# Kernel optimization log

Measured on AMD Instinct MI355X. Metric: run time of the kernel, lower is better.

## Reference

```python
import jax, jax.numpy as jnp
import numpy as np

EMBED = 1024
HEADS = 16
HDIM = EMBED // HEADS
B, S = 4, 2048
NEG = -1e20


def setup_inputs() -> dict:
    key = jax.random.key(0)
    ks = jax.random.split(key, 9)
    query = jax.random.normal(ks[0], (B, S, EMBED), dtype=jnp.float32)
    key_t = jax.random.normal(ks[1], (B, S, EMBED), dtype=jnp.float32)
    value = jax.random.normal(ks[2], (B, S, EMBED), dtype=jnp.float32)
    mask = jax.random.randint(ks[3], (1, 1, S, S), 0, 2, dtype=jnp.int32)
    padding = jax.random.randint(ks[4], (B, 1, 1, S), 0, 2, dtype=jnp.int32)
    sc = 1.0 / np.sqrt(EMBED)
    Wq = jax.random.normal(ks[5], (EMBED, EMBED), dtype=jnp.float32) * sc
    Wk = jax.random.normal(ks[6], (EMBED, EMBED), dtype=jnp.float32) * sc
    Wv = jax.random.normal(ks[7], (EMBED, EMBED), dtype=jnp.float32) * sc
    Wo = jax.random.normal(ks[8], (EMBED, EMBED), dtype=jnp.float32) * sc
    return {"query": query, "key": key_t, "value": value, "mask": mask,
            "padding": padding, "Wq": Wq, "Wk": Wk, "Wv": Wv, "Wo": Wo}


def reference(query, key, value, mask, padding, Wq, Wk, Wv, Wo):
    b, q_len, _ = query.shape
    k_len = key.shape[1]
    # projections (nn.Linear: x @ W^T), split into heads
    qs = (query @ Wq.T).reshape(b, q_len, HEADS, HDIM)
    ks = (key @ Wk.T).reshape(b, k_len, HEADS, HDIM)
    vs = (value @ Wv.T).reshape(b, k_len, HEADS, HDIM)
    scale = EMBED ** 0.25
    qs = qs / scale
    ks = ks / scale
    # [b, h, q, k] scores
    dot = jnp.einsum('bkhd,bqhd->bhqk', ks, qs)
    dot = jnp.where(mask == 0, NEG, dot)
    dot = jnp.where(padding == 0, NEG, dot)
    attn = jax.nn.softmax(dot, axis=-1)
    alpha = jnp.einsum('bhqk,bkhd->bqhd', attn, vs)
    out = alpha.reshape(b, q_len, EMBED) @ Wo.T
    return out
```

## Files before the change

### kernel.cpp

```cpp
#include <hip/hip_runtime.h>
#include <stdint.h>

#define B_  4
#define S_  2048
#define E_  1024
#define H_  16
#define D_  64

typedef __bf16 bf16;
typedef __bf16 bf16x4 __attribute__((ext_vector_type(4)));
typedef __bf16 bf16x8 __attribute__((ext_vector_type(8)));
typedef float  f32x4 __attribute__((ext_vector_type(4)));
typedef float  f32x16 __attribute__((ext_vector_type(16)));
typedef uint32_t u32x4 __attribute__((ext_vector_type(4)));

__device__ __forceinline__ f32x4 mfma16(bf16x8 a, bf16x8 b, f32x4 c) {
  return __builtin_amdgcn_mfma_f32_16x16x32_bf16(a, b, c, 0, 0, 0);
}
__device__ __forceinline__ f32x16 mfma32(bf16x8 a, bf16x8 b, f32x16 c) {
  return __builtin_amdgcn_mfma_f32_32x32x16_bf16(a, b, c, 0, 0, 0);
}

__device__ __forceinline__ int sw(int row, int idx) { return idx ^ ((row & 7) << 3); }

__device__ __forceinline__ void gl_lds16(const void* g, void* l) {
  __builtin_amdgcn_global_load_lds(
      (const __attribute__((address_space(1))) void*)g,
      (__attribute__((address_space(3))) void*)l, 16, 0, 0);
}

__device__ __forceinline__ uint32_t cvtpk(float lo, float hi) {
  uint32_t r;
  asm("v_cvt_pk_bf16_f32 %0, %1, %2" : "=v"(r) : "v"(lo), "v"(hi));
  return r;
}
__device__ __forceinline__ void plswap(uint32_t& a, uint32_t& b) {
  asm("v_permlane32_swap_b32 %0, %1" : "+v"(a), "+v"(b));
}

__global__ void pack_mask_kernel(const int* __restrict__ mask, uint32_t* __restrict__ mbits) {
  int idx = blockIdx.x * 256 + threadIdx.x;
  int q = idx >> 6, w = idx & 63;
  const int* p = mask + q * S_ + w * 32;
  uint32_t bits = 0;
#pragma unroll
  for (int j = 0; j < 32; j += 4) {
    int4 v = *(const int4*)(p + j);
    bits |= (v.x != 0 ? 1u : 0u) << (j + 0);
    bits |= (v.y != 0 ? 1u : 0u) << (j + 1);
    bits |= (v.z != 0 ? 1u : 0u) << (j + 2);
    bits |= (v.w != 0 ? 1u : 0u) << (j + 3);
  }
  mbits[idx] = bits;
}

__global__ void pack_pad_kernel(const int* __restrict__ pad, uint32_t* __restrict__ pbits) {
  int idx = threadIdx.x;
  int b = idx >> 6, w = idx & 63;
  const int* p = pad + b * S_ + w * 32;
  uint32_t bits = 0;
#pragma unroll
  for (int j = 0; j < 32; j += 4) {
    int4 v = *(const int4*)(p + j);
    bits |= (v.x != 0 ? 1u : 0u) << (j + 0);
    bits |= (v.y != 0 ? 1u : 0u) << (j + 1);
    bits |= (v.z != 0 ? 1u : 0u) << (j + 2);
    bits |= (v.w != 0 ? 1u : 0u) << (j + 3);
  }
  pbits[idx] = bits;
}

__global__ __launch_bounds__(256)
void expand_mask(const uint32_t* __restrict__ mbits, const uint32_t* __restrict__ pbits,
                 uint2* __restrict__ mbt) {
  int idx = blockIdx.x * 256 + threadIdx.x;
  int q = idx & 2047;
  int kt = (idx >> 11) & 31;
  int b = idx >> 16;
  uint2 r;
  r.x = mbits[q * 64 + kt * 2 + 0] & pbits[b * 64 + kt * 2 + 0];
  r.y = mbits[q * 64 + kt * 2 + 1] & pbits[b * 64 + kt * 2 + 1];
  mbt[idx] = r;
}

__global__ __launch_bounds__(256)
void cvt_act(const float* __restrict__ q, const float* __restrict__ k,
             const float* __restrict__ v, bf16* __restrict__ out) {
  const float* src = blockIdx.z == 0 ? q : (blockIdx.z == 1 ? k : v);
  size_t i = ((size_t)blockIdx.x * 256 + threadIdx.x) * 8;
  float4 a = *(const float4*)(src + i);
  float4 b = *(const float4*)(src + i + 4);
  bf16x8 o;
  o[0] = (bf16)a.x; o[1] = (bf16)a.y; o[2] = (bf16)a.z; o[3] = (bf16)a.w;
  o[4] = (bf16)b.x; o[5] = (bf16)b.y; o[6] = (bf16)b.z; o[7] = (bf16)b.w;
  *(bf16x8*)(out + (size_t)blockIdx.z * (8192ull * 1024ull) + i) = o;
}

__global__ __launch_bounds__(256)
void cvt_w(const float* __restrict__ w0, const float* __restrict__ w1,
           const float* __restrict__ w2, const float* __restrict__ w3,
           bf16* __restrict__ out, float sq, float sk) {
  int z = blockIdx.z;
  const float* src = z == 0 ? w0 : (z == 1 ? w1 : (z == 2 ? w2 : w3));
  float s = (z == 0) ? sq : ((z == 1) ? sk : 1.0f);
  size_t i = ((size_t)blockIdx.x * 256 + threadIdx.x) * 8;
  float4 a = *(const float4*)(src + i);
  float4 b = *(const float4*)(src + i + 4);
  bf16x8 o;
  o[0] = (bf16)(a.x * s); o[1] = (bf16)(a.y * s); o[2] = (bf16)(a.z * s); o[3] = (bf16)(a.w * s);
  o[4] = (bf16)(b.x * s); o[5] = (bf16)(b.y * s); o[6] = (bf16)(b.z * s); o[7] = (bf16)(b.w * s);
  *(bf16x8*)(out + (size_t)z * (1024ull * 1024ull) + i) = o;
}

struct GA { const bf16* A; const bf16* W; void* O; };

template<bool OUT_F32>
__global__ __launch_bounds__(256, 4)
void gemm_bf(GA g0, GA g1, GA g2) {
  GA g = (blockIdx.z == 0) ? g0 : ((blockIdx.z == 1) ? g1 : g2);
  const int id = blockIdx.x;
  const int brow = ((id & 7) * 8 + (id >> 6)) * 128;
  const int bcol = ((id >> 3) & 7) * 128;
  const int tid = threadIdx.x;
  const int l = tid & 63, wv = tid >> 6;
  const int lg = l >> 4, lr = l & 15;
  const int wr = wv >> 1, wc = wv & 1;
  const int sr = l >> 3, sc8 = l & 7;

  __shared__ bf16 Ls[2][128 * 64];
  bf16* As = Ls[0];
  bf16* Bs = Ls[1];

  f32x4 acc[4][4] = {};

  const bf16* Ab = g.A + (size_t)(brow + wv * 32 + sr) * E_ + (size_t)(sc8 ^ sr) * 8;
  const bf16* Bb = g.W + (size_t)(bcol + wv * 32 + sr) * E_ + (size_t)(sc8 ^ sr) * 8;
  bf16* la = As + (wv * 32) * 64;
  bf16* lb = Bs + (wv * 32) * 64;

  for (int kt = 0; kt < E_ / 64; ++kt) {
    __syncthreads();
    const bf16* a = Ab + kt * 64;
    const bf16* b = Bb + kt * 64;
#pragma unroll
    for (int i = 0; i < 4; ++i) {
      gl_lds16(a + (size_t)i * 8 * E_, la + i * 8 * 64);
      gl_lds16(b + (size_t)i * 8 * E_, lb + i * 8 * 64);
    }
    __syncthreads();
#pragma unroll
    for (int kk = 0; kk < 2; ++kk) {
      bf16x8 af[4], bfr[4];
#pragma unroll
      for (int ms = 0; ms < 4; ++ms) {
        int row = wr * 64 + ms * 16 + lr;
        af[ms] = *(const bf16x8*)&As[sw(row, row * 64 + kk * 32 + lg * 8)];
      }
#pragma unroll
      for (int ns = 0; ns < 4; ++ns) {
        int row = wc * 64 + ns * 16 + lr;
        bfr[ns] = *(const bf16x8*)&Bs[sw(row, row * 64 + kk * 32 + lg * 8)];
      }
#pragma unroll
      for (int ms = 0; ms < 4; ++ms)
#pragma unroll
        for (int ns = 0; ns < 4; ++ns)
          acc[ms][ns] = mfma16(af[ms], bfr[ns], acc[ms][ns]);
    }
  }

  if (!OUT_F32 && blockIdx.z == 2) {
    bf16* T = &Ls[0][0];
    __syncthreads();
#pragma unroll
    for (int ms = 0; ms < 4; ++ms) {
#pragma unroll
      for (int ns = 0; ns < 4; ++ns) {
        int col = wc * 64 + ns * 16 + lr;
        int rowb = wr * 64 + ms * 16 + lg * 4;
        bf16x4 hv;
#pragma unroll
        for (int r = 0; r < 4; ++r) hv[r] = (bf16)acc[ms][ns][r];
        *(bf16x4*)&T[col * 128 + (rowb ^ ((col & 7) << 3))] = hv;
      }
    }
    __syncthreads();
    int chunk = tid & 15, dl0 = tid >> 4;
#pragma unroll
    for (int pass = 0; pass < 8; ++pass) {
      int dl = pass * 16 + dl0;
      bf16x8 v = *(const bf16x8*)&T[dl * 128 + ((chunk * 8) ^ ((dl & 7) << 3))];
      int colg = bcol + dl;
      int bh2 = (brow >> 11) * 16 + (colg >> 6);
      int d = colg & 63;
      int s0 = (brow & 2047) + chunk * 8;
      *(bf16x8*)((bf16*)g.O + ((size_t)bh2 * 64 + d) * (size_t)S_ + s0) = v;
    }
    return;
  }

#pragma unroll
  for (int ms = 0; ms < 4; ++ms) {
#pragma unroll
    for (int ns = 0; ns < 4; ++ns) {
#pragma unroll
      for (int r = 0; r < 4; ++r) {
        int row = brow + wr * 64 + ms * 16 + lg * 4 + r;
        int col = bcol + wc * 64 + ns * 16 + lr;
        if constexpr (OUT_F32) ((float*)g.O)[(size_t)row * E_ + col] = acc[ms][ns][r];
        else                   ((bf16*)g.O)[(size_t)row * E_ + col] = (bf16)acc[ms][ns][r];
      }
    }
  }
}

__global__ __launch_bounds__(256, 4)
void attn_kernel(const bf16* __restrict__ Q, const bf16* __restrict__ K,
                 const bf16* __restrict__ Vt, const uint2* __restrict__ mbt,
                 bf16* __restrict__ alpha) {
  const int raw = blockIdx.x;
  const int xcd = raw & 7, slot = raw >> 3;
  const int bh = xcd * 8 + (slot >> 4), qblk = slot & 15;
  const int b = bh >> 4, h = bh & 15;
  const int tid = threadIdx.x, wv = tid >> 6, l = tid & 63;
  const int ln = l & 31, hi = l >> 5;
  const int qw = qblk * 128 + wv * 32;
  const int sr = l >> 3, sc8 = l & 7;
  const int g = (ln & 7) ^ (ln >> 3);

  __shared__ bf16 Ks[2][64 * 64];
  __shared__ bf16 Vs[2][64 * 64];

  bf16x8 qreg[4];
#pragma unroll
  for (int dc = 0; dc < 4; ++dc)
    qreg[dc] = *(const bf16x8*)(Q + (size_t)(b * S_ + qw + ln) * E_ + h * 64 + dc * 16 + hi * 8);

  bf16x8 ones;
#pragma unroll
  for (int j = 0; j < 8; ++j) ones[j] = (bf16)1.0f;

  f32x16 o[2] = {};
  f32x16 lacc = {};

  const bf16* Kb = K + (size_t)b * S_ * E_ + (size_t)h * 64;
  const bf16* Vb = Vt + (size_t)bh * 64 * S_;
  const uint2* mrow = mbt + ((size_t)b << 16) + qw + ln;

  auto stage = [&](int buf, int kt) {
#pragma unroll
    for (int op = 0; op < 2; ++op) {
      int rb = wv * 16 + op * 8;
      int cK = (sc8 ^ sr ^ ((rb >> 3) & 7)) * 8;
      gl_lds16(Kb + (size_t)(kt * 64 + rb + sr) * E_ + cK, Ks[buf] + rb * 64);
      gl_lds16(Vb + (size_t)(rb + sr) * S_ + kt * 64 + cK, Vs[buf] + rb * 64);
    }
  };

  stage(0, 0);
  __syncthreads();

  for (int kt = 0; kt < S_ / 64; ++kt) {
    const int cur = kt & 1;
    if (kt + 1 < S_ / 64) stage(cur ^ 1, kt + 1);

    f32x16 sc[2] = {};
    __builtin_amdgcn_s_setprio(1);
#pragma unroll
    for (int ct = 0; ct < 2; ++ct) {
#pragma unroll
      for (int dc = 0; dc < 4; ++dc) {
        int row = ct * 32 + ln;
        int c = (dc * 2 + hi) ^ g ^ (ct * 4);
        bf16x8 kf = *(const bf16x8*)&Ks[cur][row * 64 + c * 8];
        sc[ct] = mfma32(kf, qreg[dc], sc[ct]);
      }
    }
    __builtin_amdgcn_s_setprio(0);

    uint2 mv = mrow[kt << 11];
    uint32_t mq[2];
    mq[0] = mv.x >> (hi * 4);
    mq[1] = mv.y >> (hi * 4);

    uint32_t up[16];
#pragma unroll
    for (int ct = 0; ct < 2; ++ct) {
      float p[16];
#pragma unroll
      for (int r = 0; r < 16; ++r) {
        const int rel = (r & 3) + 8 * (r >> 2);
        float pe = __builtin_amdgcn_exp2f(sc[ct][r]);
        uint32_t keep = (uint32_t)__builtin_amdgcn_sbfe(mq[ct], rel, 1);
        p[r] = __builtin_bit_cast(float, __builtin_bit_cast(uint32_t, pe) & keep);
      }
#pragma unroll
      for (int j = 0; j < 8; ++j)
        up[ct * 8 + j] = cvtpk(p[2 * j], p[2 * j + 1]);
    }

#pragma unroll
    for (int kc = 0; kc < 4; ++kc) {
      const int ct = kc >> 1, base = ct * 8 + (kc & 1) * 4;
      plswap(up[base + 0], up[base + 2]);
      plswap(up[base + 1], up[base + 3]);
      u32x4 w = {up[base + 0], up[base + 1], up[base + 2], up[base + 3]};
      bf16x8 pf = __builtin_bit_cast(bf16x8, w);
      __builtin_amdgcn_s_setprio(1);
#pragma unroll
      for (int dt = 0; dt < 2; ++dt) {
        int row = dt * 32 + ln;
        int c = (kc * 2 + hi) ^ g ^ (dt * 4);
        bf16x8 vf = *(const bf16x8*)&Vs[cur][row * 64 + c * 8];
        o[dt] = mfma32(vf, pf, o[dt]);
      }
      lacc = mfma32(ones, pf, lacc);
      __builtin_amdgcn_s_setprio(0);
    }
    __syncthreads();
  }

  float inv = 1.0f / lacc[0];
  size_t qoff = (size_t)(b * S_ + qw + ln) * E_ + h * 64;
#pragma unroll
  for (int dt = 0; dt < 2; ++dt) {
#pragma unroll
    for (int rg = 0; rg < 4; ++rg) {
      bf16x4 ov;
#pragma unroll
      for (int j = 0; j < 4; ++j) ov[j] = (bf16)(o[dt][rg * 4 + j] * inv);
      *(bf16x4*)(alpha + qoff + dt * 32 + rg * 8 + hi * 4) = ov;
    }
  }
}

extern "C" void kernel_launch(void* const* d_in, const int* in_sizes, int n_in,
                              void* d_out, int out_size, void* d_ws, size_t ws_size,
                              hipStream_t stream) {
  const float* query = (const float*)d_in[0];
  const float* key_t = (const float*)d_in[1];
  const float* value = (const float*)d_in[2];
  const int*   mask  = (const int*)d_in[3];
  const int*   pad   = (const int*)d_in[4];
  const float* Wq    = (const float*)d_in[5];
  const float* Wk    = (const float*)d_in[6];
  const float* Wv    = (const float*)d_in[7];
  const float* Wo    = (const float*)d_in[8];

  char* ws = (char*)d_ws;
  bf16* Abuf  = (bf16*)ws;
  bf16* alpha = (bf16*)(ws + ((size_t)16 << 20));
  bf16* Wb    = (bf16*)(ws + ((size_t)48 << 20));
  bf16* QKV   = (bf16*)(ws + ((size_t)56 << 20));
  uint32_t* mbits = (uint32_t*)(ws + ((size_t)104 << 20));
  uint32_t* pbits = mbits + (size_t)S_ * 64;
  uint2*    mbt   = (uint2*)(ws + ((size_t)105 << 20));

  const size_t AM = 8192ull * 1024ull;
  const size_t WM = 1024ull * 1024ull;
  bf16* Vt = QKV + 2 * AM;

  pack_mask_kernel<<<512, 256, 0, stream>>>(mask, mbits);
  pack_pad_kernel<<<1, 256, 0, stream>>>(pad, pbits);
  expand_mask<<<1024, 256, 0, stream>>>(mbits, pbits, mbt);

  cvt_act<<<dim3(4096, 1, 3), 256, 0, stream>>>(query, key_t, value, Abuf);
  const float qscale = 0.17677669529663687f;
  const float log2e  = 1.4426950408889634f;
  cvt_w<<<dim3(512, 1, 4), 256, 0, stream>>>(Wq, Wk, Wv, Wo, Wb, qscale * log2e, qscale);

  GA gq{Abuf,          Wb,          QKV};
  GA gk{Abuf + AM,     Wb + WM,     QKV + AM};
  GA gv{Abuf + 2 * AM, Wb + 2 * WM, Vt};
  gemm_bf<false><<<dim3(512, 1, 3), 256, 0, stream>>>(gq, gk, gv);

  attn_kernel<<<1024, 256, 0, stream>>>(QKV, QKV + AM, Vt, mbt, alpha);

  GA go{alpha, Wb + 3 * WM, d_out};
  gemm_bf<true><<<dim3(512, 1, 1), 256, 0, stream>>>(go, go, go);
}
```

Measured before the change: 222.6 us.

## Fuse fp32-to-bf16 activation cast into QKV GEMM and split-K attention across two wave groups

Removes the separate cvt_act pass. The QKV GEMM now loads fp32 activations straight into LDS and packs them to bf16 in registers, which saves a full read and write of the bf16 copy. Attention blocks grow to 512 threads: two groups of 4 waves each handle half of the key range with 32-key tiles, and their partial outputs and row sums are combined through LDS at the end. The mask is repacked per 32-key word, and the ones-MFMA row sum is replaced by a scalar sum plus shuffle. The trade-offs are doubled LDS traffic for fp32 A tiles, lower GEMM occupancy (3 blocks), and an extra combine step.

```diff
diff --git a/kernel.cpp b/kernel.cpp
--- a/kernel.cpp
+++ b/kernel.cpp
@@ -72,28 +72,12 @@
 
 __global__ __launch_bounds__(256)
 void expand_mask(const uint32_t* __restrict__ mbits, const uint32_t* __restrict__ pbits,
-                 uint2* __restrict__ mbt) {
+                 uint32_t* __restrict__ mbt) {
   int idx = blockIdx.x * 256 + threadIdx.x;
   int q = idx & 2047;
-  int kt = (idx >> 11) & 31;
-  int b = idx >> 16;
-  uint2 r;
-  r.x = mbits[q * 64 + kt * 2 + 0] & pbits[b * 64 + kt * 2 + 0];
-  r.y = mbits[q * 64 + kt * 2 + 1] & pbits[b * 64 + kt * 2 + 1];
-  mbt[idx] = r;
-}
-
-__global__ __launch_bounds__(256)
-void cvt_act(const float* __restrict__ q, const float* __restrict__ k,
-             const float* __restrict__ v, bf16* __restrict__ out) {
-  const float* src = blockIdx.z == 0 ? q : (blockIdx.z == 1 ? k : v);
-  size_t i = ((size_t)blockIdx.x * 256 + threadIdx.x) * 8;
-  float4 a = *(const float4*)(src + i);
-  float4 b = *(const float4*)(src + i + 4);
-  bf16x8 o;
-  o[0] = (bf16)a.x; o[1] = (bf16)a.y; o[2] = (bf16)a.z; o[3] = (bf16)a.w;
-  o[4] = (bf16)b.x; o[5] = (bf16)b.y; o[6] = (bf16)b.z; o[7] = (bf16)b.w;
-  *(bf16x8*)(out + (size_t)blockIdx.z * (8192ull * 1024ull) + i) = o;
+  int ktw = (idx >> 11) & 63;
+  int b = idx >> 17;
+  mbt[idx] = mbits[q * 64 + ktw] & pbits[b * 64 + ktw];
 }
 
 __global__ __launch_bounds__(256)
@@ -112,10 +96,10 @@
   *(bf16x8*)(out + (size_t)z * (1024ull * 1024ull) + i) = o;
 }
 
-struct GA { const bf16* A; const bf16* W; void* O; };
-
-template<bool OUT_F32>
-__global__ __launch_bounds__(256, 4)
+struct GA { const void* A; const bf16* W; void* O; };
+
+template<bool A_F32, bool OUT_F32>
+__global__ __launch_bounds__(256, A_F32 ? 3 : 4)
 void gemm_bf(GA g0, GA g1, GA g2) {
   GA g = (blockIdx.z == 0) ? g0 : ((blockIdx.z == 1) ? g1 : g2);
   const int id = blockIdx.x;
@@ -125,27 +109,50 @@
   const int l = tid & 63, wv = tid >> 6;
   const int lg = l >> 4, lr = l & 15;
   const int wr = wv >> 1, wc = wv & 1;
+
+  __shared__ __align__(16) char smem[A_F32 ? 49152 : 32768];
+  bf16* Bs = (bf16*)(smem + (A_F32 ? 32768 : 16384));
+
+  f32x4 acc[4][4] = {};
+
   const int sr = l >> 3, sc8 = l & 7;
-
-  __shared__ bf16 Ls[2][128 * 64];
-  bf16* As = Ls[0];
-  bf16* Bs = Ls[1];
-
-  f32x4 acc[4][4] = {};
-
-  const bf16* Ab = g.A + (size_t)(brow + wv * 32 + sr) * E_ + (size_t)(sc8 ^ sr) * 8;
   const bf16* Bb = g.W + (size_t)(bcol + wv * 32 + sr) * E_ + (size_t)(sc8 ^ sr) * 8;
-  bf16* la = As + (wv * 32) * 64;
   bf16* lb = Bs + (wv * 32) * 64;
+
+  float* Asf = (float*)smem;
+  bf16*  Asb = (bf16*)smem;
+  const float* AbE = nullptr; const float* AbO = nullptr;
+  const bf16*  Abb = nullptr;
+  const int sr4 = l >> 4, sc16 = l & 15;
+  if constexpr (A_F32) {
+    const float* Af = (const float*)g.A;
+    AbE = Af + (size_t)(brow + wv * 32 + sr4) * E_ + (size_t)((sc16 ^ sr4) * 4);
+    AbO = Af + (size_t)(brow + wv * 32 + sr4) * E_ + (size_t)((sc16 ^ (4 + sr4)) * 4);
+  } else {
+    Abb = (const bf16*)g.A + (size_t)(brow + wv * 32 + sr) * E_ + (size_t)(sc8 ^ sr) * 8;
+  }
 
   for (int kt = 0; kt < E_ / 64; ++kt) {
     __syncthreads();
-    const bf16* a = Ab + kt * 64;
-    const bf16* b = Bb + kt * 64;
-#pragma unroll
-    for (int i = 0; i < 4; ++i) {
-      gl_lds16(a + (size_t)i * 8 * E_, la + i * 8 * 64);
-      gl_lds16(b + (size_t)i * 8 * E_, lb + i * 8 * 64);
+    if constexpr (A_F32) {
+      float* la = Asf + (wv * 32) * 64;
+#pragma unroll
+      for (int i = 0; i < 8; ++i) {
+        const float* src = ((i & 1) ? AbO : AbE) + (size_t)(i * 4) * E_ + kt * 64;
+        gl_lds16(src, la + (i * 4) * 64);
+      }
+    } else {
+      bf16* la = Asb + (wv * 32) * 64;
+      const bf16* a = Abb + kt * 64;
+#pragma unroll
+      for (int i = 0; i < 4; ++i)
+        gl_lds16(a + (size_t)i * 8 * E_, la + i * 8 * 64);
+    }
+    {
+      const bf16* b = Bb + kt * 64;
+#pragma unroll
+      for (int i = 0; i < 4; ++i)
+        gl_lds16(b + (size_t)i * 8 * E_, lb + i * 8 * 64);
     }
     __syncthreads();
 #pragma unroll
@@ -154,7 +161,16 @@
 #pragma unroll
       for (int ms = 0; ms < 4; ++ms) {
         int row = wr * 64 + ms * 16 + lr;
-        af[ms] = *(const bf16x8*)&As[sw(row, row * 64 + kk * 32 + lg * 8)];
+        if constexpr (A_F32) {
+          int g0c = 2 * (kk * 4 + lg);
+          f32x4 lo  = *(const f32x4*)&Asf[row * 64 + ((g0c ^ (row & 7)) * 4)];
+          f32x4 hi4 = *(const f32x4*)&Asf[row * 64 + (((g0c + 1) ^ (row & 7)) * 4)];
+          u32x4 pk = { cvtpk(lo[0], lo[1]), cvtpk(lo[2], lo[3]),
+                       cvtpk(hi4[0], hi4[1]), cvtpk(hi4[2], hi4[3]) };
+          af[ms] = __builtin_bit_cast(bf16x8, pk);
+        } else {
+          af[ms] = *(const bf16x8*)&Asb[sw(row, row * 64 + kk * 32 + lg * 8)];
+        }
       }
 #pragma unroll
       for (int ns = 0; ns < 4; ++ns) {
@@ -170,7 +186,7 @@
   }
 
   if (!OUT_F32 && blockIdx.z == 2) {
-    bf16* T = &Ls[0][0];
+    bf16* T = (bf16*)smem;
     __syncthreads();
 #pragma unroll
     for (int ms = 0; ms < 4; ++ms) {
@@ -214,9 +230,9 @@
   }
 }
 
-__global__ __launch_bounds__(256, 4)
+__global__ __launch_bounds__(512, 6)
 void attn_kernel(const bf16* __restrict__ Q, const bf16* __restrict__ K,
-                 const bf16* __restrict__ Vt, const uint2* __restrict__ mbt,
+                 const bf16* __restrict__ Vt, const uint32_t* __restrict__ mbt,
                  bf16* __restrict__ alpha) {
   const int raw = blockIdx.x;
   const int xcd = raw & 7, slot = raw >> 3;
@@ -224,84 +240,81 @@
   const int b = bh >> 4, h = bh & 15;
   const int tid = threadIdx.x, wv = tid >> 6, l = tid & 63;
   const int ln = l & 31, hi = l >> 5;
-  const int qw = qblk * 128 + wv * 32;
-  const int sr = l >> 3, sc8 = l & 7;
-  const int g = (ln & 7) ^ (ln >> 3);
-
-  __shared__ bf16 Ks[2][64 * 64];
-  __shared__ bf16 Vs[2][64 * 64];
+  const int grp = wv >> 2, wq = wv & 3;
+  const int qw = qblk * 128 + wq * 32;
+
+  __shared__ __align__(16) char smem[37888];
+  bf16* KsB = (bf16*)smem;
+  bf16* VsB = (bf16*)(smem + 16384);
+  float* comb = (float*)smem;
+  float* lsum = (float*)(smem + 36864);
 
   bf16x8 qreg[4];
 #pragma unroll
   for (int dc = 0; dc < 4; ++dc)
     qreg[dc] = *(const bf16x8*)(Q + (size_t)(b * S_ + qw + ln) * E_ + h * 64 + dc * 16 + hi * 8);
 
-  bf16x8 ones;
-#pragma unroll
-  for (int j = 0; j < 8; ++j) ones[j] = (bf16)1.0f;
-
   f32x16 o[2] = {};
-  f32x16 lacc = {};
+  float lrun = 0.f;
 
   const bf16* Kb = K + (size_t)b * S_ * E_ + (size_t)h * 64;
   const bf16* Vb = Vt + (size_t)bh * 64 * S_;
-  const uint2* mrow = mbt + ((size_t)b << 16) + qw + ln;
-
-  auto stage = [&](int buf, int kt) {
-#pragma unroll
-    for (int op = 0; op < 2; ++op) {
-      int rb = wv * 16 + op * 8;
-      int cK = (sc8 ^ sr ^ ((rb >> 3) & 7)) * 8;
-      gl_lds16(Kb + (size_t)(kt * 64 + rb + sr) * E_ + cK, Ks[buf] + rb * 64);
-      gl_lds16(Vb + (size_t)(rb + sr) * S_ + kt * 64 + cK, Vs[buf] + rb * 64);
-    }
+  const uint32_t* mrow = mbt + ((size_t)b << 17) + (qw + ln);
+
+  const int ksr = l >> 3, ksc = l & 7;
+  const int vsr = l >> 2, vsc = l & 3;
+  const int kr = wq * 8 + ksr;
+  const int dr = wq * 16 + vsr;
+
+  const bf16* Ksrc = Kb + (size_t)(grp * 1024 + kr) * E_ + (ksc ^ ksr) * 8;
+  const bf16* Vsrc = Vb + (size_t)dr * S_ + grp * 1024 + ((vsc ^ (vsr & 3)) * 8);
+
+  auto stage = [&](int buf, int t) {
+    gl_lds16(Ksrc + (size_t)(t * 32) * E_, KsB + (grp * 2 + buf) * 2048 + (wq * 8) * 64);
+    gl_lds16(Vsrc + t * 32,               VsB + (grp * 2 + buf) * 2048 + (wq * 16) * 32);
   };
 
   stage(0, 0);
   __syncthreads();
 
-  for (int kt = 0; kt < S_ / 64; ++kt) {
-    const int cur = kt & 1;
-    if (kt + 1 < S_ / 64) stage(cur ^ 1, kt + 1);
-
-    f32x16 sc[2] = {};
+  for (int t = 0; t < 32; ++t) {
+    const int cur = t & 1;
+    if (t + 1 < 32) stage(cur ^ 1, t + 1);
+    const bf16* ks = KsB + (grp * 2 + cur) * 2048;
+    const bf16* vs = VsB + (grp * 2 + cur) * 2048;
+
+    f32x16 sc = {};
     __builtin_amdgcn_s_setprio(1);
 #pragma unroll
-    for (int ct = 0; ct < 2; ++ct) {
-#pragma unroll
-      for (int dc = 0; dc < 4; ++dc) {
-        int row = ct * 32 + ln;
-        int c = (dc * 2 + hi) ^ g ^ (ct * 4);
-        bf16x8 kf = *(const bf16x8*)&Ks[cur][row * 64 + c * 8];
-        sc[ct] = mfma32(kf, qreg[dc], sc[ct]);
-      }
+    for (int dc = 0; dc < 4; ++dc) {
+      bf16x8 kf = *(const bf16x8*)&ks[ln * 64 + (((dc * 2 + hi) ^ (ln & 7)) * 8)];
+      sc = mfma32(kf, qreg[dc], sc);
     }
     __builtin_amdgcn_s_setprio(0);
 
-    uint2 mv = mrow[kt << 11];
-    uint32_t mq[2];
-    mq[0] = mv.x >> (hi * 4);
-    mq[1] = mv.y >> (hi * 4);
-
-    uint32_t up[16];
-#pragma unroll
-    for (int ct = 0; ct < 2; ++ct) {
-      float p[16];
-#pragma unroll
-      for (int r = 0; r < 16; ++r) {
-        const int rel = (r & 3) + 8 * (r >> 2);
-        float pe = __builtin_amdgcn_exp2f(sc[ct][r]);
-        uint32_t keep = (uint32_t)__builtin_amdgcn_sbfe(mq[ct], rel, 1);
-        p[r] = __builtin_bit_cast(float, __builtin_bit_cast(uint32_t, pe) & keep);
-      }
-#pragma unroll
-      for (int j = 0; j < 8; ++j)
-        up[ct * 8 + j] = cvtpk(p[2 * j], p[2 * j + 1]);
-    }
-
-#pragma unroll
-    for (int kc = 0; kc < 4; ++kc) {
-      const int ct = kc >> 1, base = ct * 8 + (kc & 1) * 4;
+    uint32_t mw = mrow[(size_t)(grp * 32 + t) << 11];
+    uint32_t mq = mw >> (hi * 4);
+
+    float p[16];
+#pragma unroll
+    for (int r = 0; r < 16; ++r) {
+      const int rel = (r & 3) + 8 * (r >> 2);
+      float pe = __builtin_amdgcn_exp2f(sc[r]);
+      uint32_t keep = (uint32_t)__builtin_amdgcn_sbfe(mq, rel, 1);
+      p[r] = __builtin_bit_cast(float, __builtin_bit_cast(uint32_t, pe) & keep);
+    }
+    float ps = ((p[0] + p[1]) + (p[2] + p[3])) + ((p[4] + p[5]) + (p[6] + p[7]))
+             + ((p[8] + p[9]) + (p[10] + p[11])) + ((p[12] + p[13]) + (p[14] + p[15]));
+    ps += __shfl_xor(ps, 32);
+    lrun += ps;
+
+    uint32_t up[8];
+#pragma unroll
+    for (int j = 0; j < 8; ++j) up[j] = cvtpk(p[2 * j], p[2 * j + 1]);
+
+#pragma unroll
+    for (int kc = 0; kc < 2; ++kc) {
+      const int base = kc * 4;
       plswap(up[base + 0], up[base + 2]);
       plswap(up[base + 1], up[base + 3]);
       u32x4 w = {up[base + 0], up[base + 1], up[base + 2], up[base + 3]};
@@ -310,26 +323,48 @@
 #pragma unroll
       for (int dt = 0; dt < 2; ++dt) {
         int row = dt * 32 + ln;
-        int c = (kc * 2 + hi) ^ g ^ (dt * 4);
-        bf16x8 vf = *(const bf16x8*)&Vs[cur][row * 64 + c * 8];
+        bf16x8 vf = *(const bf16x8*)&vs[row * 32 + (((kc * 2 + hi) ^ (ln & 3)) * 8)];
         o[dt] = mfma32(vf, pf, o[dt]);
       }
-      lacc = mfma32(ones, pf, lacc);
       __builtin_amdgcn_s_setprio(0);
     }
     __syncthreads();
   }
 
-  float inv = 1.0f / lacc[0];
-  size_t qoff = (size_t)(b * S_ + qw + ln) * E_ + h * 64;
-#pragma unroll
-  for (int dt = 0; dt < 2; ++dt) {
-#pragma unroll
-    for (int rg = 0; rg < 4; ++rg) {
-      bf16x4 ov;
-#pragma unroll
-      for (int j = 0; j < 4; ++j) ov[j] = (bf16)(o[dt][rg * 4 + j] * inv);
-      *(bf16x4*)(alpha + qoff + dt * 32 + rg * 8 + hi * 4) = ov;
+  const int cslot = wq * 64 + l;
+  if (grp == 1) {
+    float* dst = comb + cslot * 36;
+#pragma unroll
+    for (int dt = 0; dt < 2; ++dt)
+#pragma unroll
+      for (int rg = 0; rg < 4; ++rg) {
+        f32x4 v = {o[dt][rg * 4 + 0], o[dt][rg * 4 + 1], o[dt][rg * 4 + 2], o[dt][rg * 4 + 3]};
+        *(f32x4*)(dst + dt * 16 + rg * 4) = v;
+      }
+    lsum[cslot] = lrun;
+  }
+  __syncthreads();
+  if (grp == 0) {
+    const float* src = comb + cslot * 36;
+#pragma unroll
+    for (int dt = 0; dt < 2; ++dt)
+#pragma unroll
+      for (int rg = 0; rg < 4; ++rg) {
+        f32x4 v = *(const f32x4*)(src + dt * 16 + rg * 4);
+#pragma unroll
+        for (int j = 0; j < 4; ++j) o[dt][rg * 4 + j] += v[j];
+      }
+    float inv = 1.0f / (lrun + lsum[cslot]);
+    size_t qoff = (size_t)(b * S_ + qw + ln) * E_ + h * 64;
+#pragma unroll
+    for (int dt = 0; dt < 2; ++dt) {
+#pragma unroll
+      for (int rg = 0; rg < 4; ++rg) {
+        bf16x4 ov;
+#pragma unroll
+        for (int j = 0; j < 4; ++j) ov[j] = (bf16)(o[dt][rg * 4 + j] * inv);
+        *(bf16x4*)(alpha + qoff + dt * 32 + rg * 8 + hi * 4) = ov;
+      }
     }
   }
 }
@@ -348,13 +383,12 @@
   const float* Wo    = (const float*)d_in[8];
 
   char* ws = (char*)d_ws;
-  bf16* Abuf  = (bf16*)ws;
-  bf16* alpha = (bf16*)(ws + ((size_t)16 << 20));
-  bf16* Wb    = (bf16*)(ws + ((size_t)48 << 20));
-  bf16* QKV   = (bf16*)(ws + ((size_t)56 << 20));
-  uint32_t* mbits = (uint32_t*)(ws + ((size_t)104 << 20));
+  bf16* alpha = (bf16*)ws;
+  bf16* Wb    = (bf16*)(ws + ((size_t)16 << 20));
+  bf16* QKV   = (bf16*)(ws + ((size_t)24 << 20));
+  uint32_t* mbits = (uint32_t*)(ws + ((size_t)72 << 20));
   uint32_t* pbits = mbits + (size_t)S_ * 64;
-  uint2*    mbt   = (uint2*)(ws + ((size_t)105 << 20));
+  uint32_t* mbt   = (uint32_t*)(ws + ((size_t)73 << 20));
 
   const size_t AM = 8192ull * 1024ull;
   const size_t WM = 1024ull * 1024ull;
@@ -362,20 +396,19 @@
 
   pack_mask_kernel<<<512, 256, 0, stream>>>(mask, mbits);
   pack_pad_kernel<<<1, 256, 0, stream>>>(pad, pbits);
-  expand_mask<<<1024, 256, 0, stream>>>(mbits, pbits, mbt);
-
-  cvt_act<<<dim3(4096, 1, 3), 256, 0, stream>>>(query, key_t, value, Abuf);
+  expand_mask<<<2048, 256, 0, stream>>>(mbits, pbits, mbt);
+
   const float qscale = 0.17677669529663687f;
   const float log2e  = 1.4426950408889634f;
   cvt_w<<<dim3(512, 1, 4), 256, 0, stream>>>(Wq, Wk, Wv, Wo, Wb, qscale * log2e, qscale);
 
-  GA gq{Abuf,          Wb,          QKV};
-  GA gk{Abuf + AM,     Wb + WM,     QKV + AM};
-  GA gv{Abuf + 2 * AM, Wb + 2 * WM, Vt};
-  gemm_bf<false><<<dim3(512, 1, 3), 256, 0, stream>>>(gq, gk, gv);
-
-  attn_kernel<<<1024, 256, 0, stream>>>(QKV, QKV + AM, Vt, mbt, alpha);
+  GA gq{query, Wb,          QKV};
+  GA gk{key_t, Wb + WM,     QKV + AM};
+  GA gv{value, Wb + 2 * WM, Vt};
+  gemm_bf<true, false><<<dim3(512, 1, 3), 256, 0, stream>>>(gq, gk, gv);
+
+  attn_kernel<<<1024, 512, 0, stream>>>(QKV, QKV + AM, Vt, mbt, alpha);
 
   GA go{alpha, Wb + 3 * WM, d_out};
-  gemm_bf<true><<<dim3(512, 1, 1), 256, 0, stream>>>(go, go, go);
-}
+  gemm_bf<false, true><<<dim3(512, 1, 1), 256, 0, stream>>>(go, go, go);
+}
```

Result: slower. 294.5 us (+32.3%).

## Fuse fp32-to-bf16 activation conversion into QKV projection GEMM

Applied to the files above, without the earlier changes.

Drops the separate cvt_act kernel. The QKV GEMM now loads fp32 activations straight into LDS with an XOR swizzle and converts them to bf16 while reading MFMA fragments. This avoids writing and rereading a 48MB bf16 copy, but doubles A-tile LDS usage (occupancy hint lowered to 3) and adds conversion work to the GEMM inner loop. The attention kernel also switches to incrementing K/V/mask pointers instead of recomputing addresses each tile.

```diff
diff --git a/kernel.cpp b/kernel.cpp
--- a/kernel.cpp
+++ b/kernel.cpp
@@ -81,19 +81,6 @@
   r.x = mbits[q * 64 + kt * 2 + 0] & pbits[b * 64 + kt * 2 + 0];
   r.y = mbits[q * 64 + kt * 2 + 1] & pbits[b * 64 + kt * 2 + 1];
   mbt[idx] = r;
-}
-
-__global__ __launch_bounds__(256)
-void cvt_act(const float* __restrict__ q, const float* __restrict__ k,
-             const float* __restrict__ v, bf16* __restrict__ out) {
-  const float* src = blockIdx.z == 0 ? q : (blockIdx.z == 1 ? k : v);
-  size_t i = ((size_t)blockIdx.x * 256 + threadIdx.x) * 8;
-  float4 a = *(const float4*)(src + i);
-  float4 b = *(const float4*)(src + i + 4);
-  bf16x8 o;
-  o[0] = (bf16)a.x; o[1] = (bf16)a.y; o[2] = (bf16)a.z; o[3] = (bf16)a.w;
-  o[4] = (bf16)b.x; o[5] = (bf16)b.y; o[6] = (bf16)b.z; o[7] = (bf16)b.w;
-  *(bf16x8*)(out + (size_t)blockIdx.z * (8192ull * 1024ull) + i) = o;
 }
 
 __global__ __launch_bounds__(256)
@@ -112,10 +99,10 @@
   *(bf16x8*)(out + (size_t)z * (1024ull * 1024ull) + i) = o;
 }
 
-struct GA { const bf16* A; const bf16* W; void* O; };
-
-template<bool OUT_F32>
-__global__ __launch_bounds__(256, 4)
+struct GA { const void* A; const bf16* W; void* O; };
+
+template<bool A_F32, bool OUT_F32>
+__global__ __launch_bounds__(256, A_F32 ? 3 : 4)
 void gemm_bf(GA g0, GA g1, GA g2) {
   GA g = (blockIdx.z == 0) ? g0 : ((blockIdx.z == 1) ? g1 : g2);
   const int id = blockIdx.x;
@@ -125,27 +112,50 @@
   const int l = tid & 63, wv = tid >> 6;
   const int lg = l >> 4, lr = l & 15;
   const int wr = wv >> 1, wc = wv & 1;
+
+  __shared__ __align__(16) char smem[A_F32 ? 49152 : 32768];
+  bf16* Bs = (bf16*)(smem + (A_F32 ? 32768 : 16384));
+
+  f32x4 acc[4][4] = {};
+
   const int sr = l >> 3, sc8 = l & 7;
-
-  __shared__ bf16 Ls[2][128 * 64];
-  bf16* As = Ls[0];
-  bf16* Bs = Ls[1];
-
-  f32x4 acc[4][4] = {};
-
-  const bf16* Ab = g.A + (size_t)(brow + wv * 32 + sr) * E_ + (size_t)(sc8 ^ sr) * 8;
   const bf16* Bb = g.W + (size_t)(bcol + wv * 32 + sr) * E_ + (size_t)(sc8 ^ sr) * 8;
-  bf16* la = As + (wv * 32) * 64;
   bf16* lb = Bs + (wv * 32) * 64;
+
+  float* Asf = (float*)smem;
+  bf16*  Asb = (bf16*)smem;
+  const float* AbE = nullptr; const float* AbO = nullptr;
+  const bf16*  Abb = nullptr;
+  const int sr4 = l >> 4, sc16 = l & 15;
+  if constexpr (A_F32) {
+    const float* Af = (const float*)g.A;
+    AbE = Af + (size_t)(brow + wv * 32 + sr4) * E_ + (size_t)((sc16 ^ sr4) * 4);
+    AbO = Af + (size_t)(brow + wv * 32 + sr4) * E_ + (size_t)((sc16 ^ (4 + sr4)) * 4);
+  } else {
+    Abb = (const bf16*)g.A + (size_t)(brow + wv * 32 + sr) * E_ + (size_t)(sc8 ^ sr) * 8;
+  }
 
   for (int kt = 0; kt < E_ / 64; ++kt) {
     __syncthreads();
-    const bf16* a = Ab + kt * 64;
-    const bf16* b = Bb + kt * 64;
-#pragma unroll
-    for (int i = 0; i < 4; ++i) {
-      gl_lds16(a + (size_t)i * 8 * E_, la + i * 8 * 64);
-      gl_lds16(b + (size_t)i * 8 * E_, lb + i * 8 * 64);
+    if constexpr (A_F32) {
+      float* la = Asf + (wv * 32) * 64;
+#pragma unroll
+      for (int i = 0; i < 8; ++i) {
+        const float* src = ((i & 1) ? AbO : AbE) + (size_t)(i * 4) * E_ + kt * 64;
+        gl_lds16(src, la + (i * 4) * 64);
+      }
+    } else {
+      bf16* la = Asb + (wv * 32) * 64;
+      const bf16* a = Abb + kt * 64;
+#pragma unroll
+      for (int i = 0; i < 4; ++i)
+        gl_lds16(a + (size_t)i * 8 * E_, la + i * 8 * 64);
+    }
+    {
+      const bf16* b = Bb + kt * 64;
+#pragma unroll
+      for (int i = 0; i < 4; ++i)
+        gl_lds16(b + (size_t)i * 8 * E_, lb + i * 8 * 64);
     }
     __syncthreads();
 #pragma unroll
@@ -154,7 +164,16 @@
 #pragma unroll
       for (int ms = 0; ms < 4; ++ms) {
         int row = wr * 64 + ms * 16 + lr;
-        af[ms] = *(const bf16x8*)&As[sw(row, row * 64 + kk * 32 + lg * 8)];
+        if constexpr (A_F32) {
+          int g0c = 2 * (kk * 4 + lg);
+          f32x4 lo  = *(const f32x4*)&Asf[row * 64 + ((g0c ^ (row & 7)) * 4)];
+          f32x4 hi4 = *(const f32x4*)&Asf[row * 64 + (((g0c + 1) ^ (row & 7)) * 4)];
+          u32x4 pk = { cvtpk(lo[0], lo[1]), cvtpk(lo[2], lo[3]),
+                       cvtpk(hi4[0], hi4[1]), cvtpk(hi4[2], hi4[3]) };
+          af[ms] = __builtin_bit_cast(bf16x8, pk);
+        } else {
+          af[ms] = *(const bf16x8*)&Asb[sw(row, row * 64 + kk * 32 + lg * 8)];
+        }
       }
 #pragma unroll
       for (int ns = 0; ns < 4; ++ns) {
@@ -170,7 +189,7 @@
   }
 
   if (!OUT_F32 && blockIdx.z == 2) {
-    bf16* T = &Ls[0][0];
+    bf16* T = (bf16*)smem;
     __syncthreads();
 #pragma unroll
     for (int ms = 0; ms < 4; ++ms) {
@@ -243,26 +262,31 @@
   f32x16 o[2] = {};
   f32x16 lacc = {};
 
-  const bf16* Kb = K + (size_t)b * S_ * E_ + (size_t)h * 64;
-  const bf16* Vb = Vt + (size_t)bh * 64 * S_;
+  const int c0 = (sc8 ^ sr ^ ((wv * 2) & 7)) * 8;
+  const int c1 = (sc8 ^ sr ^ ((wv * 2 + 1) & 7)) * 8;
+  const bf16* kp0 = K + (size_t)(b * S_ + wv * 16 + sr) * E_ + h * 64 + c0;
+  const bf16* kp1 = K + (size_t)(b * S_ + wv * 16 + 8 + sr) * E_ + h * 64 + c1;
+  const bf16* vp0 = Vt + ((size_t)bh * 64 + wv * 16 + sr) * S_ + c0;
+  const bf16* vp1 = Vt + ((size_t)bh * 64 + wv * 16 + 8 + sr) * S_ + c1;
   const uint2* mrow = mbt + ((size_t)b << 16) + qw + ln;
 
-  auto stage = [&](int buf, int kt) {
-#pragma unroll
-    for (int op = 0; op < 2; ++op) {
-      int rb = wv * 16 + op * 8;
-      int cK = (sc8 ^ sr ^ ((rb >> 3) & 7)) * 8;
-      gl_lds16(Kb + (size_t)(kt * 64 + rb + sr) * E_ + cK, Ks[buf] + rb * 64);
-      gl_lds16(Vb + (size_t)(rb + sr) * S_ + kt * 64 + cK, Vs[buf] + rb * 64);
-    }
+  auto stage = [&](int buf) {
+    gl_lds16(kp0, Ks[buf] + (wv * 16) * 64);
+    gl_lds16(kp1, Ks[buf] + (wv * 16 + 8) * 64);
+    gl_lds16(vp0, Vs[buf] + (wv * 16) * 64);
+    gl_lds16(vp1, Vs[buf] + (wv * 16 + 8) * 64);
+    kp0 += (size_t)64 * E_;
+    kp1 += (size_t)64 * E_;
+    vp0 += 64;
+    vp1 += 64;
   };
 
-  stage(0, 0);
+  stage(0);
   __syncthreads();
 
-  for (int kt = 0; kt < S_ / 64; ++kt) {
+  for (int kt = 0; kt < 32; ++kt) {
     const int cur = kt & 1;
-    if (kt + 1 < S_ / 64) stage(cur ^ 1, kt + 1);
+    if (kt < 31) stage(cur ^ 1);
 
     f32x16 sc[2] = {};
     __builtin_amdgcn_s_setprio(1);
@@ -278,7 +302,8 @@
     }
     __builtin_amdgcn_s_setprio(0);
 
-    uint2 mv = mrow[kt << 11];
+    uint2 mv = *mrow;
+    mrow += 2048;
     uint32_t mq[2];
     mq[0] = mv.x >> (hi * 4);
     mq[1] = mv.y >> (hi * 4);
@@ -348,13 +373,12 @@
   const float* Wo    = (const float*)d_in[8];
 
   char* ws = (char*)d_ws;
-  bf16* Abuf  = (bf16*)ws;
-  bf16* alpha = (bf16*)(ws + ((size_t)16 << 20));
-  bf16* Wb    = (bf16*)(ws + ((size_t)48 << 20));
-  bf16* QKV   = (bf16*)(ws + ((size_t)56 << 20));
-  uint32_t* mbits = (uint32_t*)(ws + ((size_t)104 << 20));
+  bf16* alpha = (bf16*)ws;
+  bf16* Wb    = (bf16*)(ws + ((size_t)16 << 20));
+  bf16* QKV   = (bf16*)(ws + ((size_t)24 << 20));
+  uint32_t* mbits = (uint32_t*)(ws + ((size_t)72 << 20));
   uint32_t* pbits = mbits + (size_t)S_ * 64;
-  uint2*    mbt   = (uint2*)(ws + ((size_t)105 << 20));
+  uint2*    mbt   = (uint2*)(ws + ((size_t)73 << 20));
 
   const size_t AM = 8192ull * 1024ull;
   const size_t WM = 1024ull * 1024ull;
@@ -364,18 +388,17 @@
   pack_pad_kernel<<<1, 256, 0, stream>>>(pad, pbits);
   expand_mask<<<1024, 256, 0, stream>>>(mbits, pbits, mbt);
 
-  cvt_act<<<dim3(4096, 1, 3), 256, 0, stream>>>(query, key_t, value, Abuf);
   const float qscale = 0.17677669529663687f;
   const float log2e  = 1.4426950408889634f;
   cvt_w<<<dim3(512, 1, 4), 256, 0, stream>>>(Wq, Wk, Wv, Wo, Wb, qscale * log2e, qscale);
 
-  GA gq{Abuf,          Wb,          QKV};
-  GA gk{Abuf + AM,     Wb + WM,     QKV + AM};
-  GA gv{Abuf + 2 * AM, Wb + 2 * WM, Vt};
-  gemm_bf<false><<<dim3(512, 1, 3), 256, 0, stream>>>(gq, gk, gv);
+  GA gq{query, Wb,          QKV};
+  GA gk{key_t, Wb + WM,     QKV + AM};
+  GA gv{value, Wb + 2 * WM, Vt};
+  gemm_bf<true, false><<<dim3(512, 1, 3), 256, 0, stream>>>(gq, gk, gv);
 
   attn_kernel<<<1024, 256, 0, stream>>>(QKV, QKV + AM, Vt, mbt, alpha);
 
   GA go{alpha, Wb + 3 * WM, d_out};
-  gemm_bf<true><<<dim3(512, 1, 1), 256, 0, stream>>>(go, go, go);
-}
+  gemm_bf<false, true><<<dim3(512, 1, 1), 256, 0, stream>>>(go, go, go);
+}
```

Measured after the change: 208.2 us. -6.5%, faster.
